# Optimization experiments

Measured on AMD Instinct MI355X. Metric: run time of the kernel, lower is better.

## Reference

```python
import jax, jax.numpy as jnp
import numpy as np

B, N_PER, K = 8, 4096, 16          # graphs, nodes per graph, knn neighbors
D_IN, D_H, D_OUT = 32, 64, 128     # feature_nn: 35->64->64, global_nn: 64->128
N = B * N_PER


def setup_inputs() -> dict:
    key = jax.random.key(0)
    ks = jax.random.split(key, 8)
    sc = lambda fan: 1.0 / np.sqrt(fan)
    x = jax.random.normal(ks[0], (N, D_IN), jnp.float32)
    pos = jax.random.normal(ks[1], (N, 3), jnp.float32)
    batch = jnp.repeat(jnp.arange(B, dtype=jnp.int32), N_PER)
    fW1 = jax.random.normal(ks[2], (D_IN + 3, D_H), jnp.float32) * sc(D_IN + 3)
    fb1 = jnp.zeros((D_H,), jnp.float32)
    fW2 = jax.random.normal(ks[3], (D_H, D_H), jnp.float32) * sc(D_H)
    fb2 = jnp.zeros((D_H,), jnp.float32)
    gW = jax.random.normal(ks[4], (D_H, D_OUT), jnp.float32) * sc(D_H)
    gb = jnp.zeros((D_OUT,), jnp.float32)
    return {"x": x, "pos": pos, "batch": batch,
            "fW1": fW1, "fb1": fb1, "fW2": fW2, "fb2": fb2,
            "gW": gW, "gb": gb}


def reference(x, pos, batch, fW1, fb1, fW2, fb2, gW, gb):
    # ---- knn(pos, pos, k, batch, batch): per-graph k nearest (self included) ----
    posb = pos.reshape(B, N_PER, 3)
    sq = jnp.sum(posb * posb, axis=-1)                      # [B, Nper]
    dist = sq[:, :, None] + sq[:, None, :] - 2.0 * jnp.einsum('bnd,bmd->bnm', posb, posb)
    _, nbr = jax.lax.top_k(-dist, K)                        # [B, Nper, K] local neighbor idx
    offs = (jnp.arange(B, dtype=nbr.dtype) * N_PER)[:, None, None]
    col = (nbr + offs).reshape(-1)                          # edge_index[1]: neighbor (x) idx
    row = jnp.repeat(jnp.arange(N, dtype=col.dtype), K)     # edge_index[0]: query (y) idx

    # ---- PointConv: msg = feature_nn(cat[x_j, pos_j - pos_i]), max-aggregate at i ----
    # PyG flow source_to_target: j = edge_index[0] = row (query), i = edge_index[1] = col.
    msg = jnp.concatenate([x[row], pos[row] - pos[col]], axis=1)  # [E, 35]
    h = jax.nn.relu(msg @ fW1 + fb1)
    h = jax.nn.relu(h @ fW2 + fb2)                          # [E, 64]
    agg = jax.ops.segment_max(h, col, num_segments=N)       # max aggregation
    agg = jnp.where(jnp.isfinite(agg), agg, 0.0)            # PyG fills empty segments with 0
    out = jax.nn.relu(agg @ gW + gb)                        # global_nn
    return (out, pos, batch)
```

## Files before the change

kernel.cpp:

```cpp
#include <hip/hip_runtime.h>
#include <hip/hip_bf16.h>

#define N_PER    4096
#define KNBR     16
#define NTOT     32768
#define D_IN     32
#define D_H      64
#define D_OUT    128
#define E_TOT    (NTOT * KNBR)

#define OUT1_OFF (NTOT * D_OUT)
#define OUT2_OFF (NTOT * D_OUT + NTOT*3)

#define KNN_INF    3.4e38f
#define KNN_MARGIN 4e-3f

typedef __attribute__((ext_vector_type(8)))  short bf16x8;
typedef __attribute__((ext_vector_type(4)))  float f32x4;
typedef __attribute__((ext_vector_type(16))) float f32x16;

__device__ float          g_posf[NTOT * 3];
__device__ float          g_scf[NTOT];
__device__ __attribute__((aligned(16))) unsigned short g_knnA[NTOT * 16];
__device__ __attribute__((aligned(16))) unsigned short g_knnB[NTOT * 16];
__device__ int            g_nbr[E_TOT];
__device__ unsigned short g_base1h[NTOT * D_H];
__device__ uint4          g_Bfrag[2 * 4 * 64];
__device__ float          g_Wd[3 * D_H];
__device__ float          g_fb2v[D_H];
__device__ int            g_cnt[NTOT];
__device__ int            g_bsum[NTOT / 256];
__device__ int            g_offs[NTOT + 1];
__device__ int            g_cursor[NTOT];
__device__ int            g_inlist[E_TOT];
__device__ float          g_agg[NTOT * D_H];

__device__ __forceinline__ float ldf(const void* p, int i, int bf) {
    if (bf) return __uint_as_float(((unsigned)((const unsigned short*)p)[i]) << 16);
    return ((const float*)p)[i];
}
__device__ __forceinline__ unsigned bf16rne(float f) {
    unsigned u = __float_as_uint(f);
    return (u + 0x7FFFu + ((u >> 16) & 1u)) >> 16;
}
__device__ __forceinline__ void stf(void* p, int i, float v, int bf) {
    if (bf) ((unsigned short*)p)[i] = (unsigned short)bf16rne(v);
    else    ((float*)p)[i] = v;
}
__device__ __forceinline__ float b2f(unsigned short h) {
    return __uint_as_float(((unsigned)h) << 16);
}
__device__ __forceinline__ int wave_probe(const void* x) {
    unsigned wv = ((const unsigned*)x)[threadIdx.x & 63];
    unsigned e = (wv >> 7) & 0xFFu;
    unsigned long long mk = __ballot(e >= 110u && e <= 140u);
    return (__popcll(mk) >= 32) ? 1 : 0;
}

__global__ __launch_bounds__(256) void prep_kernel(const void* __restrict__ x,
                                                   const void* __restrict__ pos,
                                                   const void* __restrict__ fW1,
                                                   const void* __restrict__ fb1,
                                                   const void* __restrict__ fW2,
                                                   const void* __restrict__ fb2) {
    const int bf = wave_probe(x);
    const int b = blockIdx.x;
    if (b < 1024) {
        const int i0 = b * 256 + threadIdx.x;
        const int stride = 1024 * 256;
        for (int i = i0; i < NTOT * 3; i += stride) g_posf[i] = ldf(pos, i, bf);
        {
#pragma clang fp contract(off)
            for (int i = i0; i < NTOT; i += stride) {
                float a  = ldf(pos, i * 3 + 0, bf);
                float c2 = ldf(pos, i * 3 + 1, bf);
                float c3 = ldf(pos, i * 3 + 2, bf);
                float sc = a * a + c2 * c2 + c3 * c3;
                g_scf[i] = sc;
                g_cnt[i] = 0;
                unsigned hx = bf16rne(a),  hy = bf16rne(c2), hz = bf16rne(c3);
                float fhx = b2f(hx), fhy = b2f(hy), fhz = b2f(hz);
                unsigned lx = bf16rne(a - fhx), ly = bf16rne(c2 - fhy), lz = bf16rne(c3 - fhz);
                unsigned sch = bf16rne(sc);
                unsigned scl = bf16rne(sc - b2f(sch));
                unsigned nx = bf16rne(-2.0f * fhx), ny = bf16rne(-2.0f * fhy), nz = bf16rne(-2.0f * fhz);
                unsigned ox = bf16rne(-2.0f * b2f(lx)), oy = bf16rne(-2.0f * b2f(ly)), oz = bf16rne(-2.0f * b2f(lz));
                const unsigned ONEB = 0x3F80u;
                uint4 A0 = make_uint4(nx | (ny << 16), nz | (ox << 16), oy | (oz << 16), nx | (ny << 16));
                uint4 A1 = make_uint4(nz | (ONEB << 16), ONEB, 0u, 0u);
                uint4 B0 = make_uint4(hx | (hy << 16), hz | (hx << 16), hy | (hz << 16), lx | (ly << 16));
                uint4 B1 = make_uint4(lz | (sch << 16), scl, 0u, 0u);
                *(uint4*)&g_knnA[(size_t)i * 16]     = A0;
                *(uint4*)&g_knnA[(size_t)i * 16 + 8] = A1;
                *(uint4*)&g_knnB[(size_t)i * 16]     = B0;
                *(uint4*)&g_knnB[(size_t)i * 16 + 8] = B1;
            }
        }
        for (int i = i0; i < NTOT * D_H; i += stride) g_agg[i] = 0.0f;
    } else if (b < 2048) {
        int lane = threadIdx.x & 63, wid = threadIdx.x >> 6;
        int n0 = (b - 1024) * 32 + wid * 8;
        float wcol[D_IN];
#pragma unroll
        for (int k = 0; k < D_IN; k++) wcol[k] = ldf(fW1, k * D_H + lane, bf);
        float bb = ldf(fb1, lane, bf);
        if (bf) {
            const unsigned short* xp = (const unsigned short*)x;
            for (int r = 0; r < 8; r++) {
                int n = n0 + r;
                const uint4* xr = (const uint4*)(xp + (size_t)n * D_IN);
                float acc = bb;
#pragma unroll
                for (int q4 = 0; q4 < 4; q4++) {
                    uint4 w4 = xr[q4];
                    unsigned ww[4] = {w4.x, w4.y, w4.z, w4.w};
#pragma unroll
                    for (int p = 0; p < 4; p++) {
                        int k = q4 * 8 + p * 2;
                        acc += __uint_as_float(ww[p] << 16) * wcol[k];
                        acc += __uint_as_float(ww[p] & 0xFFFF0000u) * wcol[k + 1];
                    }
                }
                g_base1h[(size_t)n * D_H + lane] = (unsigned short)bf16rne(acc);
            }
        } else {
            const float* xp = (const float*)x;
            for (int r = 0; r < 8; r++) {
                int n = n0 + r;
                const float4* xr = (const float4*)(xp + (size_t)n * D_IN);
                float acc = bb;
#pragma unroll
                for (int q4 = 0; q4 < 8; q4++) {
                    float4 w4 = xr[q4];
                    int k = q4 * 4;
                    acc += w4.x * wcol[k] + w4.y * wcol[k + 1] + w4.z * wcol[k + 2] + w4.w * wcol[k + 3];
                }
                g_base1h[(size_t)n * D_H + lane] = (unsigned short)bf16rne(acc);
            }
        }
    } else {
        for (int t = threadIdx.x; t < 3 * D_H; t += 256) g_Wd[t] = ldf(fW1, D_IN * D_H + t, bf);
        if (threadIdx.x < D_H) g_fb2v[threadIdx.x] = ldf(fb2, threadIdx.x, bf);
        for (int idx = threadIdx.x; idx < 512; idx += 256) {
            int lane = idx & 63, nt = (idx >> 6) & 3, ks = idx >> 8;
            int n = nt * 16 + (lane & 15);
            int k0 = ks * 32 + ((lane >> 4) << 3);
            unsigned wds[4];
#pragma unroll
            for (int jp = 0; jp < 4; jp++) {
                unsigned lo = bf16rne(ldf(fW2, (k0 + 2 * jp) * D_H + n, bf));
                unsigned hi = bf16rne(ldf(fW2, (k0 + 2 * jp + 1) * D_H + n, bf));
                wds[jp] = lo | (hi << 16);
            }
            g_Bfrag[idx] = make_uint4(wds[0], wds[1], wds[2], wds[3]);
        }
    }
}

__device__ __forceinline__ void knn_sortval4(float v[4], int lane) {
#pragma unroll
    for (int k = 2; k <= 64; k <<= 1) {
#pragma unroll
        for (int j2 = k >> 1; j2 >= 1; j2 >>= 1) {
            float pv[4];
#pragma unroll
            for (int it = 0; it < 4; it++) pv[it] = __shfl_xor(v[it], j2);
            bool keepMin = (((lane & j2) == 0) == ((lane & k) == 0));
#pragma unroll
            for (int it = 0; it < 4; it++) {
                bool tp = ((pv[it] < v[it]) == keepMin);
                v[it] = tp ? pv[it] : v[it];
            }
        }
    }
}
__device__ __forceinline__ void knn_sortpair4(float d[4], int idx[4], int lane) {
#pragma unroll
    for (int k = 2; k <= 64; k <<= 1) {
#pragma unroll
        for (int j2 = k >> 1; j2 >= 1; j2 >>= 1) {
            float pd[4];
            int   pi[4];
#pragma unroll
            for (int it = 0; it < 4; it++) pd[it] = __shfl_xor(d[it], j2);
#pragma unroll
            for (int it = 0; it < 4; it++) pi[it] = __shfl_xor(idx[it], j2);
            bool keepMin = (((lane & j2) == 0) == ((lane & k) == 0));
#pragma unroll
            for (int it = 0; it < 4; it++) {
                bool lt = (pd[it] < d[it]) || (pd[it] == d[it] && pi[it] < idx[it]);
                bool tp = (lt == keepMin);
                d[it]   = tp ? pd[it] : d[it];
                idx[it] = tp ? pi[it] : idx[it];
            }
        }
    }
}

__global__ __launch_bounds__(512) void knn_kernel() {
#pragma clang fp contract(off)
    __shared__ float          s_min[32][256];
    __shared__ float          s_T[32];
    __shared__ int            s_cnt[32];
    __shared__ unsigned short s_list[32][64];

    const int t     = threadIdx.x;
    const int lane  = t & 63;
    const int w     = t >> 6;
    const int half  = lane >> 5;
    const int col   = lane & 31;
    const int qbase = blockIdx.x * 32;
    const int cbase = (qbase >> 12) << 12;

    if (t < 32) s_cnt[t] = 0;

    const int qrow = qbase + col;
    const bf16x8 afrag = *(const bf16x8*)&g_knnA[(size_t)qrow * 16 + half * 8];
    const unsigned short* bp = g_knnB + (size_t)(cbase + w * 512 + col) * 16 + half * 8;

    const f32x16 z = {};

    float m[16];
#pragma unroll
    for (int i = 0; i < 16; i++) m[i] = KNN_INF;
    {
        bf16x8 nb0 = *(const bf16x8*)(bp + 0 * 512);
        bf16x8 nb1 = *(const bf16x8*)(bp + 1 * 512);
        bf16x8 nb2 = *(const bf16x8*)(bp + 2 * 512);
        bf16x8 nb3 = *(const bf16x8*)(bp + 3 * 512);
        for (int g = 0; g < 4; g++) {
            bf16x8 cb0 = nb0, cb1 = nb1, cb2 = nb2, cb3 = nb3;
            if (g < 3) {
                const unsigned short* np = bp + (g + 1) * 2048;
                nb0 = *(const bf16x8*)(np + 0 * 512);
                nb1 = *(const bf16x8*)(np + 1 * 512);
                nb2 = *(const bf16x8*)(np + 2 * 512);
                nb3 = *(const bf16x8*)(np + 3 * 512);
            }
            f32x16 c0 = __builtin_amdgcn_mfma_f32_32x32x16_bf16(afrag, cb0, z, 0, 0, 0);
            f32x16 c1 = __builtin_amdgcn_mfma_f32_32x32x16_bf16(afrag, cb1, z, 0, 0, 0);
            f32x16 c2 = __builtin_amdgcn_mfma_f32_32x32x16_bf16(afrag, cb2, z, 0, 0, 0);
            f32x16 c3 = __builtin_amdgcn_mfma_f32_32x32x16_bf16(afrag, cb3, z, 0, 0, 0);
#pragma unroll
            for (int i = 0; i < 16; i++)
                m[i] = fminf(fminf(fminf(c0[i], c1[i]), c2[i]), fminf(c3[i], m[i]));
        }
    }
#pragma unroll
    for (int i = 0; i < 16; i++) {
        int row = (i & 3) + 8 * (i >> 2) + 4 * half;
        s_min[row][w * 32 + col] = m[i];
    }
    __syncthreads();

    {
        float tv[4];
#pragma unroll
        for (int it = 0; it < 4; it++) {
            int q = w * 4 + it;
            tv[it] = fminf(fminf(s_min[q][lane], s_min[q][64 + lane]),
                           fminf(s_min[q][128 + lane], s_min[q][192 + lane]));
        }
        knn_sortval4(tv, lane);
        if (lane == 15) {
#pragma unroll
            for (int it = 0; it < 4; it++) s_T[w * 4 + it] = tv[it] + KNN_MARGIN;
        }
    }
    __syncthreads();

    float Treg[16];
#pragma unroll
    for (int i = 0; i < 16; i++) {
        int row = (i & 3) + 8 * (i >> 2) + 4 * half;
        Treg[i] = s_T[row];
    }
    {
        bf16x8 nb0 = *(const bf16x8*)(bp + 0 * 512);
        bf16x8 nb1 = *(const bf16x8*)(bp + 1 * 512);
        bf16x8 nb2 = *(const bf16x8*)(bp + 2 * 512);
        bf16x8 nb3 = *(const bf16x8*)(bp + 3 * 512);
        for (int g = 0; g < 4; g++) {
            bf16x8 cb[4] = {nb0, nb1, nb2, nb3};
            if (g < 3) {
                const unsigned short* np = bp + (g + 1) * 2048;
                nb0 = *(const bf16x8*)(np + 0 * 512);
                nb1 = *(const bf16x8*)(np + 1 * 512);
                nb2 = *(const bf16x8*)(np + 2 * 512);
                nb3 = *(const bf16x8*)(np + 3 * 512);
            }
#pragma unroll
            for (int u = 0; u < 4; u++) {
                f32x16 c = __builtin_amdgcn_mfma_f32_32x32x16_bf16(afrag, cb[u], z, 0, 0, 0);
                int lc = w * 512 + (g * 4 + u) * 32 + col;
#pragma unroll
                for (int i = 0; i < 16; i++) {
                    if (c[i] <= Treg[i]) {
                        int q = (i & 3) + 8 * (i >> 2) + 4 * half;
                        int slot = atomicAdd(&s_cnt[q], 1);
                        if (slot < 64) s_list[q][slot] = (unsigned short)lc;
                    }
                }
            }
        }
    }
    __syncthreads();

    {
        float d4[4];
        int   idx4[4], S4[4];
#pragma unroll
        for (int it = 0; it < 4; it++) {
            int ql = w * 4 + it;
            S4[it]  = s_cnt[ql];
            idx4[it] = 0x7FFFFFFF;
            d4[it]   = KNN_INF;
            if (S4[it] <= 64 && lane < S4[it]) {
                int q  = qbase + ql;
                float qx = g_posf[q * 3 + 0], qy = g_posf[q * 3 + 1], qz = g_posf[q * 3 + 2];
                float qs = g_scf[q];
                int idx = cbase + (int)s_list[ql][lane];
                idx4[it] = idx;
                float px = g_posf[idx * 3], py = g_posf[idx * 3 + 1], pz = g_posf[idx * 3 + 2];
                float sc = g_scf[idx];
                float dot = px * qx + py * qy + pz * qz;
                d4[it] = (qs + sc) - 2.0f * dot;
            }
        }
        knn_sortpair4(d4, idx4, lane);
#pragma unroll
        for (int it = 0; it < 4; it++) {
            int q = qbase + w * 4 + it;
            if (S4[it] <= 64) {
                if (lane < 16) {
                    g_nbr[q * KNBR + lane] = idx4[it];
                    atomicAdd(&g_cnt[idx4[it] & (NTOT - 1)], 1);
                }
            } else {
                const float* cp  = g_posf + cbase * 3;
                const float* csc = g_scf + cbase;
                float qx = g_posf[q * 3 + 0], qy = g_posf[q * 3 + 1], qz = g_posf[q * 3 + 2];
                float qs = g_scf[q];
                float lastd = -KNN_INF; int lasti = -1;
                for (int t16 = 0; t16 < 16; t16++) {
                    float bd = KNN_INF; int bi = 0x7FFFFFFF;
                    for (int cc = 0; cc < 64; cc++) {
                        int jj = cc * 64 + lane;
                        float px = cp[jj * 3], py = cp[jj * 3 + 1], pz = cp[jj * 3 + 2];
                        float sc = csc[jj];
                        float dot = px * qx + py * qy + pz * qz;
                        float dd = (qs + sc) - 2.0f * dot;
                        int gj = cbase + jj;
                        bool after  = (dd > lastd) || (dd == lastd && gj > lasti);
                        bool better = (dd < bd) || (dd == bd && gj < bi);
                        if (after && better) { bd = dd; bi = gj; }
                    }
#pragma unroll
                    for (int s2 = 1; s2 < 64; s2 <<= 1) {
                        float od = __shfl_xor(bd, s2);
                        int   oi = __shfl_xor(bi, s2);
                        if (od < bd || (od == bd && oi < bi)) { bd = od; bi = oi; }
                    }
                    if (lane == 0) {
                        g_nbr[q * KNBR + t16] = bi;
                        atomicAdd(&g_cnt[bi & (NTOT - 1)], 1);
                    }
                    lastd = bd; lasti = bi;
                }
            }
        }
    }
}

__global__ __launch_bounds__(256) void scanA_kernel() {
    __shared__ int red[4];
    int t = threadIdx.x, lane = t & 63, w = t >> 6;
    int v = g_cnt[blockIdx.x * 256 + t];
    int s = v;
#pragma unroll
    for (int off = 1; off < 64; off <<= 1) s += __shfl_xor(s, off);
    if (lane == 0) red[w] = s;
    __syncthreads();
    if (t == 0) g_bsum[blockIdx.x] = red[0] + red[1] + red[2] + red[3];
}

__global__ __launch_bounds__(256) void scanC_kernel() {
    __shared__ int sred[4];
    __shared__ int wsum[4];
    int t = threadIdx.x, lane = t & 63, w = t >> 6;
    int contrib = (t < 128 && t < blockIdx.x) ? g_bsum[t] : 0;
    int rs = contrib;
#pragma unroll
    for (int off = 1; off < 64; off <<= 1) rs += __shfl_xor(rs, off);
    if (lane == 0) sred[w] = rs;
    __syncthreads();
    int base = sred[0] + sred[1] + sred[2] + sred[3];

    int i = blockIdx.x * 256 + t;
    int v = g_cnt[i];
    int inc = v;
#pragma unroll
    for (int off = 1; off < 64; off <<= 1) {
        int u = __shfl_up(inc, off);
        if (lane >= off) inc += u;
    }
    if (lane == 63) wsum[w] = inc;
    __syncthreads();
    int wbase = 0;
    for (int k = 0; k < w; k++) wbase += wsum[k];
    int excl = base + wbase + inc - v;
    g_offs[i] = excl;
    g_cursor[i] = excl;
    if (i == NTOT - 1) g_offs[NTOT] = E_TOT;
}

__global__ void scatter_kernel() {
    int e = blockIdx.x * 256 + threadIdx.x;
    int c = g_nbr[e] & (NTOT - 1);
    int slot = atomicAdd(&g_cursor[c], 1);
    g_inlist[slot & (E_TOT - 1)] = e;
}

__global__ __launch_bounds__(256) void edge_kernel() {
    __shared__ unsigned short sA[256 * 72];
    __shared__ int scol[256];
    const int t    = threadIdx.x;
    const int lane = t & 63;
    const int w    = t >> 6;
    const int slot0 = blockIdx.x * 256;

    {
        int e = g_inlist[slot0 + t];
        int n = (e >> 4) & (NTOT - 1);
        int j = g_nbr[e] & (NTOT - 1);
        scol[t] = j;
        float dx = g_posf[n * 3 + 0] - g_posf[j * 3 + 0];
        float dy = g_posf[n * 3 + 1] - g_posf[j * 3 + 1];
        float dz = g_posf[n * 3 + 2] - g_posf[j * 3 + 2];
        const unsigned short* b1 = g_base1h + (size_t)n * D_H;
#pragma unroll
        for (int d0 = 0; d0 < D_H; d0 += 8) {
            uint4 p = *(const uint4*)(b1 + d0);
            unsigned pw[4] = {p.x, p.y, p.z, p.w};
            unsigned qw[4];
#pragma unroll
            for (int jp = 0; jp < 4; jp++) {
                int d = d0 + 2 * jp;
                float v0 = __uint_as_float(pw[jp] << 16)
                         + dx * g_Wd[d]     + dy * g_Wd[64 + d]     + dz * g_Wd[128 + d];
                float v1 = __uint_as_float(pw[jp] & 0xFFFF0000u)
                         + dx * g_Wd[d + 1] + dy * g_Wd[64 + d + 1] + dz * g_Wd[128 + d + 1];
                v0 = fmaxf(v0, 0.f); v1 = fmaxf(v1, 0.f);
                qw[jp] = bf16rne(v0) | (bf16rne(v1) << 16);
            }
            *(uint4*)(&sA[t * 72 + d0]) = make_uint4(qw[0], qw[1], qw[2], qw[3]);
        }
    }
    __syncthreads();

    f32x4 acc[4][4];
#pragma unroll
    for (int a = 0; a < 4; a++)
#pragma unroll
        for (int b = 0; b < 4; b++) acc[a][b] = (f32x4){0.f, 0.f, 0.f, 0.f};

    const int quad = lane >> 4;
    const int l15  = lane & 15;
#pragma unroll
    for (int ks = 0; ks < 2; ks++) {
        bf16x8 bfrag[4];
#pragma unroll
        for (int nt = 0; nt < 4; nt++)
            bfrag[nt] = ((const bf16x8*)g_Bfrag)[ks * 256 + nt * 64 + lane];
#pragma unroll
        for (int mt = 0; mt < 4; mt++) {
            int row = w * 64 + mt * 16 + l15;
            bf16x8 afrag = *(const bf16x8*)(&sA[row * 72 + ks * 32 + quad * 8]);
#pragma unroll
            for (int nt = 0; nt < 4; nt++)
                acc[mt][nt] = __builtin_amdgcn_mfma_f32_16x16x32_bf16(afrag, bfrag[nt], acc[mt][nt], 0, 0, 0);
        }
    }
    __syncthreads();

#pragma unroll
    for (int nt = 0; nt < 4; nt++) {
        int dim = nt * 16 + l15;
        float bb = g_fb2v[dim];
#pragma unroll
        for (int mt = 0; mt < 4; mt++) {
#pragma unroll
            for (int r = 0; r < 4; r++) {
                int edge = w * 64 + mt * 16 + quad * 4 + r;
                float v = fmaxf(acc[mt][nt][r] + bb, 0.f);
                sA[edge * 72 + dim] = (unsigned short)bf16rne(v);
            }
        }
    }
    __syncthreads();

    {
        const int ls0 = w * 64;
        const int gs0 = slot0 + ls0;
        int cur = -1;
        float vmax = 0.f;
        for (int s = ls0; s < ls0 + 64; s++) {
            int cj = scol[s];
            float v = b2f(sA[s * 72 + lane]);
            if (cj != cur) {
                if (cur >= 0) {
                    int lo = g_offs[cur], hi = g_offs[cur + 1];
                    if (lo >= gs0 && hi <= gs0 + 64)
                        g_agg[(size_t)cur * D_H + lane] = vmax;
                    else
                        atomicMax((unsigned*)&g_agg[(size_t)cur * D_H + lane], __float_as_uint(vmax));
                }
                cur = cj; vmax = v;
            } else {
                vmax = fmaxf(vmax, v);
            }
        }
        if (cur >= 0) {
            int lo = g_offs[cur], hi = g_offs[cur + 1];
            if (lo >= gs0 && hi <= gs0 + 64)
                g_agg[(size_t)cur * D_H + lane] = vmax;
            else
                atomicMax((unsigned*)&g_agg[(size_t)cur * D_H + lane], __float_as_uint(vmax));
        }
    }
}

__global__ __launch_bounds__(256) void outmisc_kernel(const void* __restrict__ x,
                                                      const void* __restrict__ gW,
                                                      const void* __restrict__ gb,
                                                      const int* __restrict__ batch,
                                                      const void* __restrict__ pos,
                                                      void* __restrict__ out) {
    const int bf = wave_probe(x);
    const int b = blockIdx.x;
    if (b < 2048) {
        int t = threadIdx.x, d = t & 127, half = t >> 7;
        float gcol[D_H];
#pragma unroll
        for (int k = 0; k < D_H; k++) gcol[k] = ldf(gW, k * D_OUT + d, bf);
        float bb = ldf(gb, d, bf);
        int n0 = b * 16 + half * 8;
        for (int r = 0; r < 8; r++) {
            int n = n0 + r;
            float acc = bb;
#pragma unroll
            for (int k = 0; k < D_H; k++) acc += g_agg[(size_t)n * D_H + k] * gcol[k];
            stf(out, n * D_OUT + d, fmaxf(acc, 0.f), bf);
        }
    } else {
        int i = (b - 2048) * 256 + threadIdx.x;
        if (bf) {
            if (i < NTOT * 3) ((unsigned short*)out)[OUT1_OFF + i] = ((const unsigned short*)pos)[i];
            if (i < NTOT)     ((unsigned short*)out)[OUT2_OFF + i] = (unsigned short)bf16rne((float)batch[i]);
        } else {
            if (i < NTOT * 3) ((float*)out)[OUT1_OFF + i] = ((const float*)pos)[i];
            if (i < NTOT)     ((float*)out)[OUT2_OFF + i] = (float)batch[i];
        }
    }
}

extern "C" void kernel_launch(void* const* d_in, const int* in_sizes, int n_in,
                              void* d_out, int out_size, void* d_ws, size_t ws_size,
                              hipStream_t stream) {
    const void* x     = d_in[0];
    const void* pos   = d_in[1];
    const int*  batch = (const int*)d_in[2];
    const void* fW1   = d_in[3];
    const void* fb1   = d_in[4];
    const void* fW2   = d_in[5];
    const void* fb2   = d_in[6];
    const void* gW    = d_in[7];
    const void* gb    = d_in[8];

    hipLaunchKernelGGL(prep_kernel,    dim3(2049),        dim3(256), 0, stream, x, pos, fW1, fb1, fW2, fb2);
    hipLaunchKernelGGL(knn_kernel,     dim3(NTOT / 32),   dim3(512), 0, stream);
    hipLaunchKernelGGL(scanA_kernel,   dim3(NTOT / 256),  dim3(256), 0, stream);
    hipLaunchKernelGGL(scanC_kernel,   dim3(NTOT / 256),  dim3(256), 0, stream);
    hipLaunchKernelGGL(scatter_kernel, dim3(E_TOT / 256), dim3(256), 0, stream);
    hipLaunchKernelGGL(edge_kernel,    dim3(E_TOT / 256), dim3(256), 0, stream);
    hipLaunchKernelGGL(outmisc_kernel, dim3(2048 + (NTOT * 3 + 255) / 256), dim3(256), 0, stream,
                       x, gW, gb, batch, pos, d_out);
}
```

Before: 272.2 us.

## Switch KNN distance MFMA from 32x32x16 to 16x16x32 tiles

Replaces the 32x32x16 bf16 MFMA distance tiles in the KNN kernel with pairs of 16x16x32 MFMAs covering the two 16-query halves. The K=16 feature dimension is zero-padded to 32, so half the lanes load zeros. This cuts the per-lane accumulator and min/threshold register count from 16 to 8 and halves the per-wave shared min buffer. In exchange it wastes half of each MFMA's K depth on padding and issues twice as many MFMA instructions with smaller outputs.

```diff
diff --git a/kernel.cpp b/kernel.cpp
--- a/kernel.cpp
+++ b/kernel.cpp
@@ -199,7 +199,7 @@
 
 __global__ __launch_bounds__(512) void knn_kernel() {
 #pragma clang fp contract(off)
-    __shared__ float          s_min[32][256];
+    __shared__ float          s_min[32][128];
     __shared__ float          s_T[32];
     __shared__ int            s_cnt[32];
     __shared__ unsigned short s_list[32][64];
@@ -207,49 +207,60 @@
     const int t     = threadIdx.x;
     const int lane  = t & 63;
     const int w     = t >> 6;
-    const int half  = lane >> 5;
-    const int col   = lane & 31;
+    const int quad  = lane >> 4;
+    const int cq    = lane & 15;
     const int qbase = blockIdx.x * 32;
     const int cbase = (qbase >> 12) << 12;
 
     if (t < 32) s_cnt[t] = 0;
 
-    const int qrow = qbase + col;
-    const bf16x8 afrag = *(const bf16x8*)&g_knnA[(size_t)qrow * 16 + half * 8];
-    const unsigned short* bp = g_knnB + (size_t)(cbase + w * 512 + col) * 16 + half * 8;
-
-    const f32x16 z = {};
-
-    float m[16];
-#pragma unroll
-    for (int i = 0; i < 16; i++) m[i] = KNN_INF;
+    const bf16x8 zf = {};
+    bf16x8 af0 = zf, af1 = zf;
+    if (quad < 2) {
+        af0 = *(const bf16x8*)&g_knnA[(size_t)(qbase + cq) * 16 + quad * 8];
+        af1 = *(const bf16x8*)&g_knnA[(size_t)(qbase + 16 + cq) * 16 + quad * 8];
+    }
+    const unsigned short* bp = g_knnB + (size_t)(cbase + w * 512 + cq) * 16 + quad * 8;
+
+    const f32x4 z4 = {};
+
+    float m8[8];
+#pragma unroll
+    for (int i = 0; i < 8; i++) m8[i] = KNN_INF;
     {
-        bf16x8 nb0 = *(const bf16x8*)(bp + 0 * 512);
-        bf16x8 nb1 = *(const bf16x8*)(bp + 1 * 512);
-        bf16x8 nb2 = *(const bf16x8*)(bp + 2 * 512);
-        bf16x8 nb3 = *(const bf16x8*)(bp + 3 * 512);
-        for (int g = 0; g < 4; g++) {
+        bf16x8 nb0 = zf, nb1 = zf, nb2 = zf, nb3 = zf;
+        if (quad < 2) {
+            nb0 = *(const bf16x8*)(bp + 0 * 256);
+            nb1 = *(const bf16x8*)(bp + 1 * 256);
+            nb2 = *(const bf16x8*)(bp + 2 * 256);
+            nb3 = *(const bf16x8*)(bp + 3 * 256);
+        }
+        for (int g = 0; g < 8; g++) {
             bf16x8 cb0 = nb0, cb1 = nb1, cb2 = nb2, cb3 = nb3;
-            if (g < 3) {
-                const unsigned short* np = bp + (g + 1) * 2048;
-                nb0 = *(const bf16x8*)(np + 0 * 512);
-                nb1 = *(const bf16x8*)(np + 1 * 512);
-                nb2 = *(const bf16x8*)(np + 2 * 512);
-                nb3 = *(const bf16x8*)(np + 3 * 512);
-            }
-            f32x16 c0 = __builtin_amdgcn_mfma_f32_32x32x16_bf16(afrag, cb0, z, 0, 0, 0);
-            f32x16 c1 = __builtin_amdgcn_mfma_f32_32x32x16_bf16(afrag, cb1, z, 0, 0, 0);
-            f32x16 c2 = __builtin_amdgcn_mfma_f32_32x32x16_bf16(afrag, cb2, z, 0, 0, 0);
-            f32x16 c3 = __builtin_amdgcn_mfma_f32_32x32x16_bf16(afrag, cb3, z, 0, 0, 0);
-#pragma unroll
-            for (int i = 0; i < 16; i++)
-                m[i] = fminf(fminf(fminf(c0[i], c1[i]), c2[i]), fminf(c3[i], m[i]));
-        }
-    }
-#pragma unroll
-    for (int i = 0; i < 16; i++) {
-        int row = (i & 3) + 8 * (i >> 2) + 4 * half;
-        s_min[row][w * 32 + col] = m[i];
+            if (g < 7 && quad < 2) {
+                const unsigned short* np = bp + (g + 1) * 1024;
+                nb0 = *(const bf16x8*)(np + 0 * 256);
+                nb1 = *(const bf16x8*)(np + 1 * 256);
+                nb2 = *(const bf16x8*)(np + 2 * 256);
+                nb3 = *(const bf16x8*)(np + 3 * 256);
+            }
+#pragma unroll
+            for (int u = 0; u < 4; u++) {
+                bf16x8 cb = (u == 0) ? cb0 : (u == 1) ? cb1 : (u == 2) ? cb2 : cb3;
+                f32x4 c0 = __builtin_amdgcn_mfma_f32_16x16x32_bf16(af0, cb, z4, 0, 0, 0);
+                f32x4 c1 = __builtin_amdgcn_mfma_f32_16x16x32_bf16(af1, cb, z4, 0, 0, 0);
+#pragma unroll
+                for (int j = 0; j < 4; j++) {
+                    m8[j]     = fminf(m8[j], c0[j]);
+                    m8[4 + j] = fminf(m8[4 + j], c1[j]);
+                }
+            }
+        }
+    }
+#pragma unroll
+    for (int j = 0; j < 4; j++) {
+        s_min[quad * 4 + j][w * 16 + cq]      = m8[j];
+        s_min[16 + quad * 4 + j][w * 16 + cq] = m8[4 + j];
     }
     __syncthreads();
 
@@ -258,8 +269,7 @@
 #pragma unroll
         for (int it = 0; it < 4; it++) {
             int q = w * 4 + it;
-            tv[it] = fminf(fminf(s_min[q][lane], s_min[q][64 + lane]),
-                           fminf(s_min[q][128 + lane], s_min[q][192 + lane]));
+            tv[it] = fminf(s_min[q][lane], s_min[q][64 + lane]);
         }
         knn_sortval4(tv, lane);
         if (lane == 15) {
@@ -269,34 +279,44 @@
     }
     __syncthreads();
 
-    float Treg[16];
-#pragma unroll
-    for (int i = 0; i < 16; i++) {
-        int row = (i & 3) + 8 * (i >> 2) + 4 * half;
-        Treg[i] = s_T[row];
+    float Treg[8];
+#pragma unroll
+    for (int j = 0; j < 4; j++) {
+        Treg[j]     = s_T[quad * 4 + j];
+        Treg[4 + j] = s_T[16 + quad * 4 + j];
     }
     {
-        bf16x8 nb0 = *(const bf16x8*)(bp + 0 * 512);
-        bf16x8 nb1 = *(const bf16x8*)(bp + 1 * 512);
-        bf16x8 nb2 = *(const bf16x8*)(bp + 2 * 512);
-        bf16x8 nb3 = *(const bf16x8*)(bp + 3 * 512);
-        for (int g = 0; g < 4; g++) {
-            bf16x8 cb[4] = {nb0, nb1, nb2, nb3};
-            if (g < 3) {
-                const unsigned short* np = bp + (g + 1) * 2048;
-                nb0 = *(const bf16x8*)(np + 0 * 512);
-                nb1 = *(const bf16x8*)(np + 1 * 512);
-                nb2 = *(const bf16x8*)(np + 2 * 512);
-                nb3 = *(const bf16x8*)(np + 3 * 512);
+        bf16x8 nb0 = zf, nb1 = zf, nb2 = zf, nb3 = zf;
+        if (quad < 2) {
+            nb0 = *(const bf16x8*)(bp + 0 * 256);
+            nb1 = *(const bf16x8*)(bp + 1 * 256);
+            nb2 = *(const bf16x8*)(bp + 2 * 256);
+            nb3 = *(const bf16x8*)(bp + 3 * 256);
+        }
+        for (int g = 0; g < 8; g++) {
+            bf16x8 cb0 = nb0, cb1 = nb1, cb2 = nb2, cb3 = nb3;
+            if (g < 7 && quad < 2) {
+                const unsigned short* np = bp + (g + 1) * 1024;
+                nb0 = *(const bf16x8*)(np + 0 * 256);
+                nb1 = *(const bf16x8*)(np + 1 * 256);
+                nb2 = *(const bf16x8*)(np + 2 * 256);
+                nb3 = *(const bf16x8*)(np + 3 * 256);
             }
 #pragma unroll
             for (int u = 0; u < 4; u++) {
-                f32x16 c = __builtin_amdgcn_mfma_f32_32x32x16_bf16(afrag, cb[u], z, 0, 0, 0);
-                int lc = w * 512 + (g * 4 + u) * 32 + col;
-#pragma unroll
-                for (int i = 0; i < 16; i++) {
-                    if (c[i] <= Treg[i]) {
-                        int q = (i & 3) + 8 * (i >> 2) + 4 * half;
+                bf16x8 cb = (u == 0) ? cb0 : (u == 1) ? cb1 : (u == 2) ? cb2 : cb3;
+                f32x4 c0 = __builtin_amdgcn_mfma_f32_16x16x32_bf16(af0, cb, z4, 0, 0, 0);
+                f32x4 c1 = __builtin_amdgcn_mfma_f32_16x16x32_bf16(af1, cb, z4, 0, 0, 0);
+                int lc = w * 512 + (g * 4 + u) * 16 + cq;
+#pragma unroll
+                for (int j = 0; j < 4; j++) {
+                    if (c0[j] <= Treg[j]) {
+                        int q = quad * 4 + j;
+                        int slot = atomicAdd(&s_cnt[q], 1);
+                        if (slot < 64) s_list[q][slot] = (unsigned short)lc;
+                    }
+                    if (c1[j] <= Treg[4 + j]) {
+                        int q = 16 + quad * 4 + j;
                         int slot = atomicAdd(&s_cnt[q], 1);
                         if (slot < 64) s_list[q][slot] = (unsigned short)lc;
                     }
```

Measured after the change: 315.1 us. +15.8%, slower.

## Replace global-atomic counting sort with per-graph LDS bucket kernel

Applied to the files above, without the earlier changes.

Drops the global atomic neighbor counting in the knn kernel and replaces the scanA, scanC and scatter kernels with one per-graph kernel. That kernel builds a histogram in shared memory, scans it, and scatters edges into the CSR inlist using LDS atomics. This removes two kernel launches, the global atomic traffic, and the cross-block scan. In exchange it runs only 8 blocks of 1024 threads, which uses a small share of the GPU and could become a serial bottleneck.

```diff
diff --git a/kernel.cpp b/kernel.cpp
--- a/kernel.cpp
+++ b/kernel.cpp
@@ -28,10 +28,7 @@
 __device__ uint4          g_Bfrag[2 * 4 * 64];
 __device__ float          g_Wd[3 * D_H];
 __device__ float          g_fb2v[D_H];
-__device__ int            g_cnt[NTOT];
-__device__ int            g_bsum[NTOT / 256];
 __device__ int            g_offs[NTOT + 1];
-__device__ int            g_cursor[NTOT];
 __device__ int            g_inlist[E_TOT];
 __device__ float          g_agg[NTOT * D_H];
 
@@ -77,7 +74,6 @@
                 float c3 = ldf(pos, i * 3 + 2, bf);
                 float sc = a * a + c2 * c2 + c3 * c3;
                 g_scf[i] = sc;
-                g_cnt[i] = 0;
                 unsigned hx = bf16rne(a),  hy = bf16rne(c2), hz = bf16rne(c3);
                 float fhx = b2f(hx), fhy = b2f(hy), fhz = b2f(hz);
                 unsigned lx = bf16rne(a - fhx), ly = bf16rne(c2 - fhy), lz = bf16rne(c3 - fhz);
@@ -334,7 +330,6 @@
             if (S4[it] <= 64) {
                 if (lane < 16) {
                     g_nbr[q * KNBR + lane] = idx4[it];
-                    atomicAdd(&g_cnt[idx4[it] & (NTOT - 1)], 1);
                 }
             } else {
                 const float* cp  = g_posf + cbase * 3;
@@ -363,7 +358,6 @@
                     }
                     if (lane == 0) {
                         g_nbr[q * KNBR + t16] = bi;
-                        atomicAdd(&g_cnt[bi & (NTOT - 1)], 1);
                     }
                     lastd = bd; lasti = bi;
                 }
@@ -372,53 +366,55 @@
     }
 }
 
-__global__ __launch_bounds__(256) void scanA_kernel() {
-    __shared__ int red[4];
-    int t = threadIdx.x, lane = t & 63, w = t >> 6;
-    int v = g_cnt[blockIdx.x * 256 + t];
-    int s = v;
-#pragma unroll
-    for (int off = 1; off < 64; off <<= 1) s += __shfl_xor(s, off);
-    if (lane == 0) red[w] = s;
-    __syncthreads();
-    if (t == 0) g_bsum[blockIdx.x] = red[0] + red[1] + red[2] + red[3];
-}
-
-__global__ __launch_bounds__(256) void scanC_kernel() {
-    __shared__ int sred[4];
-    __shared__ int wsum[4];
-    int t = threadIdx.x, lane = t & 63, w = t >> 6;
-    int contrib = (t < 128 && t < blockIdx.x) ? g_bsum[t] : 0;
-    int rs = contrib;
-#pragma unroll
-    for (int off = 1; off < 64; off <<= 1) rs += __shfl_xor(rs, off);
-    if (lane == 0) sred[w] = rs;
-    __syncthreads();
-    int base = sred[0] + sred[1] + sred[2] + sred[3];
-
-    int i = blockIdx.x * 256 + t;
-    int v = g_cnt[i];
-    int inc = v;
+__global__ __launch_bounds__(1024) void bucket_kernel() {
+    __shared__ int h[N_PER];
+    __shared__ int wsum[16];
+    const int g    = blockIdx.x;
+    const int t    = threadIdx.x;
+    const int lane = t & 63;
+    const int wv   = t >> 6;
+    const int ebase = g * (N_PER * KNBR);
+    const int nbase = g * N_PER;
+
+    for (int i = t; i < N_PER; i += 1024) h[i] = 0;
+    __syncthreads();
+
+    for (int i = t; i < N_PER * KNBR; i += 1024) {
+        int c = g_nbr[ebase + i] & (N_PER - 1);
+        atomicAdd(&h[c], 1);
+    }
+    __syncthreads();
+
+    int a0 = h[4 * t], a1 = h[4 * t + 1], a2 = h[4 * t + 2], a3 = h[4 * t + 3];
+    int s = a0 + a1 + a2 + a3;
+    int inc = s;
 #pragma unroll
     for (int off = 1; off < 64; off <<= 1) {
         int u = __shfl_up(inc, off);
         if (lane >= off) inc += u;
     }
-    if (lane == 63) wsum[w] = inc;
+    if (lane == 63) wsum[wv] = inc;
     __syncthreads();
     int wbase = 0;
-    for (int k = 0; k < w; k++) wbase += wsum[k];
-    int excl = base + wbase + inc - v;
-    g_offs[i] = excl;
-    g_cursor[i] = excl;
-    if (i == NTOT - 1) g_offs[NTOT] = E_TOT;
-}
-
-__global__ void scatter_kernel() {
-    int e = blockIdx.x * 256 + threadIdx.x;
-    int c = g_nbr[e] & (NTOT - 1);
-    int slot = atomicAdd(&g_cursor[c], 1);
-    g_inlist[slot & (E_TOT - 1)] = e;
+    for (int k = 0; k < wv; k++) wbase += wsum[k];
+    int e0 = wbase + inc - s;
+    g_offs[nbase + 4 * t + 0] = ebase + e0;
+    g_offs[nbase + 4 * t + 1] = ebase + e0 + a0;
+    g_offs[nbase + 4 * t + 2] = ebase + e0 + a0 + a1;
+    g_offs[nbase + 4 * t + 3] = ebase + e0 + a0 + a1 + a2;
+    h[4 * t + 0] = e0;
+    h[4 * t + 1] = e0 + a0;
+    h[4 * t + 2] = e0 + a0 + a1;
+    h[4 * t + 3] = e0 + a0 + a1 + a2;
+    if (g == 7 && t == 1023) g_offs[NTOT] = E_TOT;
+    __syncthreads();
+
+    for (int i = t; i < N_PER * KNBR; i += 1024) {
+        int e = ebase + i;
+        int c = g_nbr[e] & (N_PER - 1);
+        int slot = atomicAdd(&h[c], 1);
+        g_inlist[ebase + slot] = e;
+    }
 }
 
 __global__ __launch_bounds__(256) void edge_kernel() {
@@ -577,12 +573,10 @@
     const void* gW    = d_in[7];
     const void* gb    = d_in[8];
 
-    hipLaunchKernelGGL(prep_kernel,    dim3(2049),        dim3(256), 0, stream, x, pos, fW1, fb1, fW2, fb2);
-    hipLaunchKernelGGL(knn_kernel,     dim3(NTOT / 32),   dim3(512), 0, stream);
-    hipLaunchKernelGGL(scanA_kernel,   dim3(NTOT / 256),  dim3(256), 0, stream);
-    hipLaunchKernelGGL(scanC_kernel,   dim3(NTOT / 256),  dim3(256), 0, stream);
-    hipLaunchKernelGGL(scatter_kernel, dim3(E_TOT / 256), dim3(256), 0, stream);
-    hipLaunchKernelGGL(edge_kernel,    dim3(E_TOT / 256), dim3(256), 0, stream);
+    hipLaunchKernelGGL(prep_kernel,    dim3(2049),        dim3(256),  0, stream, x, pos, fW1, fb1, fW2, fb2);
+    hipLaunchKernelGGL(knn_kernel,     dim3(NTOT / 32),   dim3(512),  0, stream);
+    hipLaunchKernelGGL(bucket_kernel,  dim3(8),           dim3(1024), 0, stream);
+    hipLaunchKernelGGL(edge_kernel,    dim3(E_TOT / 256), dim3(256),  0, stream);
     hipLaunchKernelGGL(outmisc_kernel, dim3(2048 + (NTOT * 3 + 255) / 256), dim3(256), 0, stream,
                        x, gW, gb, batch, pos, d_out);
 }
```

Result: slower. 290.9 us (+6.9%).

## Replace global-atomic CSR build with per-graph LDS histogram and block-local scatter

Applied to the files above, without the earlier changes.

Removes the per-edge global atomicAdd on neighbor counts from the kNN kernel and computes counts in a new hist_kernel, where 64 blocks (8 per graph) each build a 4096-bin LDS histogram and keep their partial histograms. The scatter step now uses per-block LDS cursors seeded from the scan offsets plus the partial histograms of earlier blocks, replacing global atomics on a cursor array. This cuts global atomic contention but adds a kernel launch and runs each phase on only 64 blocks, which may underuse the GPU. Insertion order within each bucket becomes deterministic per block.

```diff
diff --git a/kernel.cpp b/kernel.cpp
--- a/kernel.cpp
+++ b/kernel.cpp
@@ -31,7 +31,7 @@
 __device__ int            g_cnt[NTOT];
 __device__ int            g_bsum[NTOT / 256];
 __device__ int            g_offs[NTOT + 1];
-__device__ int            g_cursor[NTOT];
+__device__ int            g_phist[64 * N_PER];
 __device__ int            g_inlist[E_TOT];
 __device__ float          g_agg[NTOT * D_H];
 
@@ -334,7 +334,6 @@
             if (S4[it] <= 64) {
                 if (lane < 16) {
                     g_nbr[q * KNBR + lane] = idx4[it];
-                    atomicAdd(&g_cnt[idx4[it] & (NTOT - 1)], 1);
                 }
             } else {
                 const float* cp  = g_posf + cbase * 3;
@@ -363,12 +362,37 @@
                     }
                     if (lane == 0) {
                         g_nbr[q * KNBR + t16] = bi;
-                        atomicAdd(&g_cnt[bi & (NTOT - 1)], 1);
                     }
                     lastd = bd; lasti = bi;
                 }
             }
         }
+    }
+}
+
+__global__ __launch_bounds__(256) void hist_kernel() {
+    __shared__ int h[N_PER];
+    const int b = blockIdx.x;
+    const int g = b >> 3;
+    const int ebase = g * (N_PER * KNBR) + (b & 7) * 8192;
+    const int t = threadIdx.x;
+
+    for (int i = t; i < N_PER; i += 256) h[i] = 0;
+    __syncthreads();
+
+    for (int i0 = 0; i0 < 8192; i0 += 2048) {
+        int v[8];
+#pragma unroll
+        for (int u = 0; u < 8; u++) v[u] = g_nbr[ebase + i0 + u * 256 + t] & (N_PER - 1);
+#pragma unroll
+        for (int u = 0; u < 8; u++) atomicAdd(&h[v[u]], 1);
+    }
+    __syncthreads();
+
+    for (int i = t; i < N_PER; i += 256) {
+        int hv = h[i];
+        g_phist[b * N_PER + i] = hv;
+        atomicAdd(&g_cnt[g * N_PER + i], hv);
     }
 }
 
@@ -410,15 +434,37 @@
     for (int k = 0; k < w; k++) wbase += wsum[k];
     int excl = base + wbase + inc - v;
     g_offs[i] = excl;
-    g_cursor[i] = excl;
     if (i == NTOT - 1) g_offs[NTOT] = E_TOT;
 }
 
-__global__ void scatter_kernel() {
-    int e = blockIdx.x * 256 + threadIdx.x;
-    int c = g_nbr[e] & (NTOT - 1);
-    int slot = atomicAdd(&g_cursor[c], 1);
-    g_inlist[slot & (E_TOT - 1)] = e;
+__global__ __launch_bounds__(256) void scatter2_kernel() {
+    __shared__ int cur[N_PER];
+    const int b = blockIdx.x;
+    const int g = b >> 3;
+    const int ebase = g * (N_PER * KNBR) + (b & 7) * 8192;
+    const int nbase = g * N_PER;
+    const int t = threadIdx.x;
+
+    for (int i = t; i < N_PER; i += 256) {
+        int base = g_offs[nbase + i];
+        for (int cc = (g << 3); cc < b; cc++) base += g_phist[cc * N_PER + i];
+        cur[i] = base;
+    }
+    __syncthreads();
+
+    for (int i0 = 0; i0 < 8192; i0 += 2048) {
+        int e[8], v[8];
+#pragma unroll
+        for (int u = 0; u < 8; u++) {
+            e[u] = ebase + i0 + u * 256 + t;
+            v[u] = g_nbr[e[u]] & (N_PER - 1);
+        }
+#pragma unroll
+        for (int u = 0; u < 8; u++) {
+            int slot = atomicAdd(&cur[v[u]], 1);
+            g_inlist[slot] = e[u];
+        }
+    }
 }
 
 __global__ __launch_bounds__(256) void edge_kernel() {
@@ -577,12 +623,13 @@
     const void* gW    = d_in[7];
     const void* gb    = d_in[8];
 
-    hipLaunchKernelGGL(prep_kernel,    dim3(2049),        dim3(256), 0, stream, x, pos, fW1, fb1, fW2, fb2);
-    hipLaunchKernelGGL(knn_kernel,     dim3(NTOT / 32),   dim3(512), 0, stream);
-    hipLaunchKernelGGL(scanA_kernel,   dim3(NTOT / 256),  dim3(256), 0, stream);
-    hipLaunchKernelGGL(scanC_kernel,   dim3(NTOT / 256),  dim3(256), 0, stream);
-    hipLaunchKernelGGL(scatter_kernel, dim3(E_TOT / 256), dim3(256), 0, stream);
-    hipLaunchKernelGGL(edge_kernel,    dim3(E_TOT / 256), dim3(256), 0, stream);
-    hipLaunchKernelGGL(outmisc_kernel, dim3(2048 + (NTOT * 3 + 255) / 256), dim3(256), 0, stream,
+    hipLaunchKernelGGL(prep_kernel,     dim3(2049),        dim3(256), 0, stream, x, pos, fW1, fb1, fW2, fb2);
+    hipLaunchKernelGGL(knn_kernel,      dim3(NTOT / 32),   dim3(512), 0, stream);
+    hipLaunchKernelGGL(hist_kernel,     dim3(64),          dim3(256), 0, stream);
+    hipLaunchKernelGGL(scanA_kernel,    dim3(NTOT / 256),  dim3(256), 0, stream);
+    hipLaunchKernelGGL(scanC_kernel,    dim3(NTOT / 256),  dim3(256), 0, stream);
+    hipLaunchKernelGGL(scatter2_kernel, dim3(64),          dim3(256), 0, stream);
+    hipLaunchKernelGGL(edge_kernel,     dim3(E_TOT / 256), dim3(256), 0, stream);
+    hipLaunchKernelGGL(outmisc_kernel,  dim3(2048 + (NTOT * 3 + 255) / 256), dim3(256), 0, stream,
                        x, gW, gb, batch, pos, d_out);
 }
```

Result: no change. 274.4 us (+0.8%).
